# Kernel tuning notes

Hardware: AMD Instinct MI355X
Metric: run time of the kernel (lower is better)

## Reference

```python
import jax, jax.numpy as jnp
import numpy as np

D_K = 8192   # sequence length (module calls it d_k)
D_MODEL = 128

def setup_inputs() -> dict:
    key = jax.random.key(0)
    k1, k2, k3 = jax.random.split(key, 3)
    Q = jax.random.normal(k1, (D_K, D_MODEL), dtype=jnp.float32)
    K = jax.random.normal(k2, (D_K, D_MODEL), dtype=jnp.float32)
    V = jax.random.normal(k3, (D_K, D_MODEL), dtype=jnp.float32)
    return {"Q": Q, "K": K, "V": V}

def reference(Q, K, V):
    # scores: [d_k, d_k] -- full attention matrix, scaled by 1/sqrt(d_k)
    # (faithful to the source: scale uses d_k, the sequence dim)
    inv_scale = 1.0 / jnp.sqrt(jnp.asarray(D_K, dtype=Q.dtype))
    scores = jnp.einsum('qd,kd->qk', Q, K) * inv_scale
    attn = jax.nn.softmax(scores, axis=-1)
    return jnp.einsum('qk,kd->qd', attn, V)
```

## Files before the change

kernel.cpp:

```cpp
#include <hip/hip_runtime.h>

#define SEQ 8192
#define DM  128
#define KS  16

typedef __attribute__((ext_vector_type(8)))  short bf16x8;
typedef __attribute__((ext_vector_type(16))) float f32x16;
typedef __attribute__((ext_vector_type(2)))  unsigned int uintx2;

static __device__ __forceinline__ unsigned short f2bf(float f) {
    unsigned int u = __builtin_bit_cast(unsigned int, f);
    u += 0x7FFFu + ((u >> 16) & 1u);
    return (unsigned short)(u >> 16);
}
static __device__ __forceinline__ unsigned int pack2bf(float a, float b) {
    return ((unsigned int)f2bf(b) << 16) | (unsigned int)f2bf(a);
}
static __device__ __forceinline__ float bflo(unsigned int u) {
    return __builtin_bit_cast(float, u << 16);
}
static __device__ __forceinline__ float bfhi(unsigned int u) {
    return __builtin_bit_cast(float, u & 0xFFFF0000u);
}
static __device__ __forceinline__ bf16x8 as_frag(uint4 v) {
    return __builtin_bit_cast(bf16x8, v);
}
static __device__ __forceinline__ unsigned int pack2bf_trunc(float a, float b) {
    return __builtin_amdgcn_perm(__builtin_bit_cast(unsigned int, b),
                                 __builtin_bit_cast(unsigned int, a), 0x07060302u);
}
static __device__ __forceinline__ void gl_lds16(const void* g, void* l) {
    __builtin_amdgcn_global_load_lds(
        (const __attribute__((address_space(1))) void*)(unsigned long long)g,
        (__attribute__((address_space(3))) void*)(unsigned int)(unsigned long long)l,
        16, 0, 0);
}
#define CL2 (1.4426950408889634f / 90.50966799187809f)

__global__ __launch_bounds__(512) void prep_kernel(
        const float* __restrict__ Q, const float* __restrict__ K,
        const float* __restrict__ V,
        uint2* __restrict__ Qb2, uint4* __restrict__ Kt, uint4* __restrict__ Vt) {
    __shared__ float VL[32 * 132 + 4];
    const int b = blockIdx.x, tid = threadIdx.x;
    const float4* Q4 = (const float4*)Q;
    const float4* K4 = (const float4*)K;
    const float4* V4 = (const float4*)V;

    #pragma unroll
    for (int u = 0; u < 2; ++u) {
        int f4 = u * 512 + tid;
        int k = f4 >> 5, c4 = f4 & 31;
        float4 v = V4[(size_t)b * 1024 + f4];
        *(float4*)(VL + k * 132 + c4 * 4) = v;
    }
    #pragma unroll
    for (int u = 0; u < 2; ++u) {
        int f4 = u * 512 + tid;
        float4 v = Q4[(size_t)b * 1024 + f4];
        Qb2[(size_t)b * 1024 + f4] = make_uint2(pack2bf(v.x * CL2, v.y * CL2),
                                                pack2bf(v.z * CL2, v.w * CL2));
    }
    {
        int p = tid;
        int q = p & 31, h = (p >> 5) & 1, s = p >> 6;
        int fi = (b * 32 + q) * 32 + s * 4 + h * 2;
        float4 a = K4[fi], c = K4[fi + 1];
        Kt[(size_t)b * 512 + p] = make_uint4(pack2bf(a.x, a.y), pack2bf(a.z, a.w),
                                             pack2bf(c.x, c.y), pack2bf(c.z, c.w));
    }
    __syncthreads();
    {
        int p = tid;
        int q = p & 31, h = (p >> 5) & 1, w = p >> 6;
        int d = (w >> 1) * 32 + q;
        int k0 = (w & 1) * 16 + h * 8;
        unsigned int r[4];
        #pragma unroll
        for (int jj = 0; jj < 4; ++jj) {
            float e0 = VL[(k0 + 2 * jj) * 132 + d];
            float e1 = VL[(k0 + 2 * jj + 1) * 132 + d];
            r[jj] = pack2bf(e0, e1);
        }
        Vt[(size_t)b * 512 + p] = make_uint4(r[0], r[1], r[2], r[3]);
    }
}

__global__ __launch_bounds__(256, 2) void attn_kernel(
        const unsigned short* __restrict__ Qb,
        const uint4* __restrict__ Kt,
        const uint4* __restrict__ Vt,
        uint2* __restrict__ Opart, float* __restrict__ Lpart) {
    __shared__ __align__(16) char smem[32768];
    const int tid = threadIdx.x;
    const int wid = tid >> 6, lane = tid & 63;
    const int i = wid;
    const int q = lane & 31, h = lane >> 5;
    const int qt = blockIdx.x & 63, ks = blockIdx.x >> 6;
    const int qbase = qt * 128 + i * 32;
    const int tile0 = ks * 16;

    uint4 qf[8];
    {
        const unsigned short* qrow = Qb + (qbase + q) * DM + 8 * h;
        #pragma unroll
        for (int s = 0; s < 8; ++s) qf[s] = *(const uint4*)(qrow + 16 * s);
    }

    f32x16 oacc[4];
    #pragma unroll
    for (int mb = 0; mb < 4; ++mb)
        #pragma unroll
        for (int r = 0; r < 16; ++r) oacc[mb][r] = 0.f;
    float ls0 = 0.f, ls1 = 0.f, ls2 = 0.f, ls3 = 0.f;

    auto stage = [&](int buf, int tile) {
        char* base = smem + buf * 16384;
        const uint4* kt = Kt + (size_t)tile * 512;
        const uint4* vt = Vt + (size_t)tile * 512;
        #pragma unroll
        for (int u = 0; u < 2; ++u) {
            int ki = i * 2 + u;
            gl_lds16(kt + ki * 64 + lane, base + ki * 1024);
            gl_lds16(vt + ki * 64 + lane, base + 8192 + ki * 1024);
        }
    };

    stage(0, tile0);
    #pragma unroll 1
    for (int t = 0; t < 16; ++t) {
        __syncthreads();
        if (t < 15) stage((t + 1) & 1, tile0 + t + 1);
        const char* kl = smem + (t & 1) * 16384 + lane * 16;

        uint4 kf[8];
        #pragma unroll
        for (int s = 0; s < 8; ++s) kf[s] = *(const uint4*)(kl + s * 1024);

        f32x16 sa, sb;
        #pragma unroll
        for (int r = 0; r < 16; ++r) { sa[r] = 0.f; sb[r] = 0.f; }
        __builtin_amdgcn_s_setprio(1);
        #pragma unroll
        for (int s = 0; s < 4; ++s) {
            sa = __builtin_amdgcn_mfma_f32_32x32x16_bf16(
                     as_frag(kf[s]), as_frag(qf[s]), sa, 0, 0, 0);
            sb = __builtin_amdgcn_mfma_f32_32x32x16_bf16(
                     as_frag(kf[s + 4]), as_frag(qf[s + 4]), sb, 0, 0, 0);
        }
        __builtin_amdgcn_s_setprio(0);

        uint4 vf[8];
        #pragma unroll
        for (int w = 0; w < 8; ++w) vf[w] = *(const uint4*)(kl + 8192 + w * 1024);

        float p[16];
        #pragma unroll
        for (int r = 0; r < 16; ++r) p[r] = __builtin_amdgcn_exp2f(sa[r] + sb[r]);
        #pragma unroll
        for (int r = 0; r < 4; ++r) {
            ls0 += p[4 * r + 0]; ls1 += p[4 * r + 1];
            ls2 += p[4 * r + 2]; ls3 += p[4 * r + 3];
        }
        unsigned int pk[8];
        #pragma unroll
        for (int jj = 0; jj < 8; ++jj) pk[jj] = pack2bf_trunc(p[2 * jj], p[2 * jj + 1]);
        uint4 B0, B1;
        {
            uintx2 r0 = __builtin_amdgcn_permlane32_swap(pk[0], pk[2], false, false);
            uintx2 r1 = __builtin_amdgcn_permlane32_swap(pk[1], pk[3], false, false);
            uintx2 r4 = __builtin_amdgcn_permlane32_swap(pk[4], pk[6], false, false);
            uintx2 r5 = __builtin_amdgcn_permlane32_swap(pk[5], pk[7], false, false);
            B0.x = r0[0];  B0.z = r0[1];
            B0.y = r1[0];  B0.w = r1[1];
            B1.x = r4[0];  B1.z = r4[1];
            B1.y = r5[0];  B1.w = r5[1];
        }

        __builtin_amdgcn_s_setprio(1);
        #pragma unroll
        for (int mb = 0; mb < 4; ++mb) {
            oacc[mb] = __builtin_amdgcn_mfma_f32_32x32x16_bf16(
                           as_frag(vf[mb * 2 + 0]), as_frag(B0), oacc[mb], 0, 0, 0);
            oacc[mb] = __builtin_amdgcn_mfma_f32_32x32x16_bf16(
                           as_frag(vf[mb * 2 + 1]), as_frag(B1), oacc[mb], 0, 0, 0);
        }
        __builtin_amdgcn_s_setprio(0);
    }
    float lsum = (ls0 + ls1) + (ls2 + ls3);

    float l2 = lsum + __shfl_xor(lsum, 32);
    if (h == 0) Lpart[(size_t)ks * SEQ + qbase + q] = l2;

    #pragma unroll
    for (int pass = 0; pass < 2; ++pass) {
        __syncthreads();
        if ((i >> 1) == pass) {
            float* Lg = (float*)(smem + (i & 1) * 16384);
            #pragma unroll
            for (int mb = 0; mb < 4; ++mb)
                #pragma unroll
                for (int r = 0; r < 16; ++r) {
                    int dl = 32 * mb + (r & 3) + 8 * (r >> 2) + 4 * h;
                    Lg[dl * 32 + q] = oacc[mb][r];
                }
        }
        __syncthreads();
        #pragma unroll
        for (int u = 0; u < 8; ++u) {
            int idx = u * 256 + tid;
            int rd = idx >> 4, c4l = idx & 15;
            int ig = c4l >> 3, q4 = c4l & 7;
            float4 v = *(const float4*)(smem + ig * 16384 + (rd * 8 + q4) * 16);
            Opart[(((size_t)(ks * 64 + qt)) * 128 + rd) * 32 + pass * 16 + c4l] =
                make_uint2(pack2bf(v.x, v.y), pack2bf(v.z, v.w));
        }
    }
}

__global__ __launch_bounds__(512) void reduce_kernel(
        const uint2* __restrict__ Opart, const float* __restrict__ Lpart,
        float* __restrict__ Out) {
    __shared__ float T[32 * 132 + 4];
    __shared__ float Rinv[128];
    const int tid = threadIdx.x;
    const int qt = blockIdx.x & 63, dq = blockIdx.x >> 6;
    if (tid < 128) {
        float L = 0.f;
        #pragma unroll
        for (int ks = 0; ks < KS; ++ks) L += Lpart[(size_t)ks * SEQ + qt * 128 + tid];
        Rinv[tid] = 1.0f / L;
    }
    const int c = tid & 31, dsub = tid >> 5;
    float4 acc[2];
    #pragma unroll
    for (int rr = 0; rr < 2; ++rr) { acc[rr].x = acc[rr].y = acc[rr].z = acc[rr].w = 0.f; }
    #pragma unroll
    for (int ks = 0; ks < KS; ++ks) {
        #pragma unroll
        for (int rr = 0; rr < 2; ++rr) {
            int d_l = rr * 16 + dsub;
            uint2 w = Opart[(((size_t)(ks * 64 + qt)) * 128 + dq * 32 + d_l) * 32 + c];
            acc[rr].x += bflo(w.x); acc[rr].y += bfhi(w.x);
            acc[rr].z += bflo(w.y); acc[rr].w += bfhi(w.y);
        }
    }
    #pragma unroll
    for (int rr = 0; rr < 2; ++rr)
        *(float4*)(T + (rr * 16 + dsub) * 132 + c * 4) = acc[rr];
    __syncthreads();
    const int q_l = tid >> 2, part = tid & 3;
    float r = Rinv[q_l];
    #pragma unroll
    for (int g = 0; g < 2; ++g) {
        int d0 = part * 8 + g * 4;
        float4 o;
        o.x = T[(d0 + 0) * 132 + q_l] * r;
        o.y = T[(d0 + 1) * 132 + q_l] * r;
        o.z = T[(d0 + 2) * 132 + q_l] * r;
        o.w = T[(d0 + 3) * 132 + q_l] * r;
        *(float4*)(Out + ((size_t)(qt * 128 + q_l)) * DM + dq * 32 + d0) = o;
    }
}

extern "C" void kernel_launch(void* const* d_in, const int* in_sizes, int n_in,
                              void* d_out, int out_size, void* d_ws, size_t ws_size,
                              hipStream_t stream) {
    const float* Q = (const float*)d_in[0];
    const float* K = (const float*)d_in[1];
    const float* V = (const float*)d_in[2];
    char* ws = (char*)d_ws;
    uint2* Qb2  = (uint2*)ws;
    uint4* Kt   = (uint4*)(ws + 2 * 1024 * 1024);
    uint4* Vt   = (uint4*)(ws + 4 * 1024 * 1024);
    float* Lpart= (float*)(ws + 6 * 1024 * 1024);
    uint2* Opart= (uint2*)(ws + 6 * 1024 * 1024 + 524288);
    float* Out  = (float*)d_out;

    prep_kernel<<<256, 512, 0, stream>>>(Q, K, V, Qb2, Kt, Vt);
    attn_kernel<<<1024, 256, 0, stream>>>((const unsigned short*)Qb2, Kt, Vt,
                                          Opart, Lpart);
    reduce_kernel<<<256, 512, 0, stream>>>(Opart, Lpart, Out);
}
```

Before: 116.7 us.

## Triple-buffer K and double-buffer V with register prefetch of next K tile

Splits the combined K/V staging into separate K (three buffers) and V (two buffers) rings in shared memory, so K is loaded two tiles ahead and V one tile ahead. The next K fragments are read into registers during the current iteration, and the barrier moves to the end of the loop. The aim is to hide global-to-LDS latency and LDS reads behind the MFMA work. In exchange, shared memory grows from 32 KB to 40 KB and register pressure rises, which could reduce occupancy.

New measurement: 119.1 us. +2.1%, slower.

```diff
diff --git a/kernel.cpp b/kernel.cpp
--- a/kernel.cpp
+++ b/kernel.cpp
@@ -91,10 +91,10 @@
         const uint4* __restrict__ Kt,
         const uint4* __restrict__ Vt,
         uint2* __restrict__ Opart, float* __restrict__ Lpart) {
-    __shared__ __align__(16) char smem[32768];
+    __shared__ __align__(16) char smem[40960];
     const int tid = threadIdx.x;
-    const int wid = tid >> 6, lane = tid & 63;
-    const int i = wid;
+    const int lane = tid & 63;
+    const int i = tid >> 6;
     const int q = lane & 31, h = lane >> 5;
     const int qt = blockIdx.x & 63, ks = blockIdx.x >> 6;
     const int qbase = qt * 128 + i * 32;
@@ -114,29 +114,42 @@
         for (int r = 0; r < 16; ++r) oacc[mb][r] = 0.f;
     float ls0 = 0.f, ls1 = 0.f, ls2 = 0.f, ls3 = 0.f;
 
-    auto stage = [&](int buf, int tile) {
-        char* base = smem + buf * 16384;
-        const uint4* kt = Kt + (size_t)tile * 512;
-        const uint4* vt = Vt + (size_t)tile * 512;
+    const uint4* const kt0 = Kt + (size_t)tile0 * 512;
+    const uint4* const vt0 = Vt + (size_t)tile0 * 512;
+
+    auto stageK = [&](int kb, const uint4* src) {
+        char* b = smem + kb * 8192;
         #pragma unroll
         for (int u = 0; u < 2; ++u) {
             int ki = i * 2 + u;
-            gl_lds16(kt + ki * 64 + lane, base + ki * 1024);
-            gl_lds16(vt + ki * 64 + lane, base + 8192 + ki * 1024);
+            gl_lds16(src + ki * 64 + lane, b + ki * 1024);
         }
     };
-
-    stage(0, tile0);
+    auto stageV = [&](int vb, const uint4* src) {
+        char* b = smem + 24576 + vb * 8192;
+        #pragma unroll
+        for (int u = 0; u < 2; ++u) {
+            int ki = i * 2 + u;
+            gl_lds16(src + ki * 64 + lane, b + ki * 1024);
+        }
+    };
+
+    stageK(0, kt0);
+    stageV(0, vt0);
+    stageK(1, kt0 + 512);
+    __syncthreads();
+
+    uint4 kfp[8];
+    #pragma unroll
+    for (int s = 0; s < 8; ++s)
+        kfp[s] = *(const uint4*)(smem + lane * 16 + s * 1024);
+
+    int kb1 = 1;
+    int kb2 = 2;
+    int vb  = 0;
+
     #pragma unroll 1
     for (int t = 0; t < 16; ++t) {
-        __syncthreads();
-        if (t < 15) stage((t + 1) & 1, tile0 + t + 1);
-        const char* kl = smem + (t & 1) * 16384 + lane * 16;
-
-        uint4 kf[8];
-        #pragma unroll
-        for (int s = 0; s < 8; ++s) kf[s] = *(const uint4*)(kl + s * 1024);
-
         f32x16 sa, sb;
         #pragma unroll
         for (int r = 0; r < 16; ++r) { sa[r] = 0.f; sb[r] = 0.f; }
@@ -144,15 +157,26 @@
         #pragma unroll
         for (int s = 0; s < 4; ++s) {
             sa = __builtin_amdgcn_mfma_f32_32x32x16_bf16(
-                     as_frag(kf[s]), as_frag(qf[s]), sa, 0, 0, 0);
+                     as_frag(kfp[s]), as_frag(qf[s]), sa, 0, 0, 0);
             sb = __builtin_amdgcn_mfma_f32_32x32x16_bf16(
-                     as_frag(kf[s + 4]), as_frag(qf[s + 4]), sb, 0, 0, 0);
+                     as_frag(kfp[s + 4]), as_frag(qf[s + 4]), sb, 0, 0, 0);
         }
         __builtin_amdgcn_s_setprio(0);
 
+        if (t < 14) stageK(kb2, kt0 + (size_t)(t + 2) * 512);
+        if (t < 15) stageV(vb ^ 1, vt0 + (size_t)(t + 1) * 512);
+
         uint4 vf[8];
-        #pragma unroll
-        for (int w = 0; w < 8; ++w) vf[w] = *(const uint4*)(kl + 8192 + w * 1024);
+        {
+            const char* vl = smem + 24576 + vb * 8192 + lane * 16;
+            #pragma unroll
+            for (int w = 0; w < 8; ++w) vf[w] = *(const uint4*)(vl + w * 1024);
+        }
+        if (t < 15) {
+            const char* kl = smem + kb1 * 8192 + lane * 16;
+            #pragma unroll
+            for (int s = 0; s < 8; ++s) kfp[s] = *(const uint4*)(kl + s * 1024);
+        }
 
         float p[16];
         #pragma unroll
@@ -186,6 +210,11 @@
                            as_frag(vf[mb * 2 + 1]), as_frag(B1), oacc[mb], 0, 0, 0);
         }
         __builtin_amdgcn_s_setprio(0);
+
+        __syncthreads();
+        kb1 = (kb1 == 2) ? 0 : kb1 + 1;
+        kb2 = (kb2 == 2) ? 0 : kb2 + 1;
+        vb ^= 1;
     }
     float lsum = (ls0 + ls1) + (ls2 + ls3);
 
```

## Load K/V tiles directly into registers with double-buffered prefetch instead of LDS

Applied to the files above, without the earlier changes.

Replaces the global-to-LDS async staging of K and V tiles, and the per-tile __syncthreads, with direct global loads into register arrays. Two register buffers (A/B) alternate, and the next-but-one tile's K and V are prefetched right after they are consumed. This removes LDS round trips and block-wide barriers, but every wave now loads the full K/V tile separately. That raises global/L2 traffic about 4x and raises VGPR pressure, which could hurt occupancy under launch_bounds(256,2).

New measurement: 177.8 us. +52.4%, slower.

```diff
diff --git a/kernel.cpp b/kernel.cpp
--- a/kernel.cpp
+++ b/kernel.cpp
@@ -28,12 +28,6 @@
 static __device__ __forceinline__ unsigned int pack2bf_trunc(float a, float b) {
     return __builtin_amdgcn_perm(__builtin_bit_cast(unsigned int, b),
                                  __builtin_bit_cast(unsigned int, a), 0x07060302u);
-}
-static __device__ __forceinline__ void gl_lds16(const void* g, void* l) {
-    __builtin_amdgcn_global_load_lds(
-        (const __attribute__((address_space(1))) void*)(unsigned long long)g,
-        (__attribute__((address_space(3))) void*)(unsigned int)(unsigned long long)l,
-        16, 0, 0);
 }
 #define CL2 (1.4426950408889634f / 90.50966799187809f)
 
@@ -93,8 +87,8 @@
         uint2* __restrict__ Opart, float* __restrict__ Lpart) {
     __shared__ __align__(16) char smem[32768];
     const int tid = threadIdx.x;
-    const int wid = tid >> 6, lane = tid & 63;
-    const int i = wid;
+    const int lane = tid & 63;
+    const int i = tid >> 6;
     const int q = lane & 31, h = lane >> 5;
     const int qt = blockIdx.x & 63, ks = blockIdx.x >> 6;
     const int qbase = qt * 128 + i * 32;
@@ -114,29 +108,16 @@
         for (int r = 0; r < 16; ++r) oacc[mb][r] = 0.f;
     float ls0 = 0.f, ls1 = 0.f, ls2 = 0.f, ls3 = 0.f;
 
-    auto stage = [&](int buf, int tile) {
-        char* base = smem + buf * 16384;
-        const uint4* kt = Kt + (size_t)tile * 512;
-        const uint4* vt = Vt + (size_t)tile * 512;
-        #pragma unroll
-        for (int u = 0; u < 2; ++u) {
-            int ki = i * 2 + u;
-            gl_lds16(kt + ki * 64 + lane, base + ki * 1024);
-            gl_lds16(vt + ki * 64 + lane, base + 8192 + ki * 1024);
-        }
-    };
-
-    stage(0, tile0);
-    #pragma unroll 1
-    for (int t = 0; t < 16; ++t) {
-        __syncthreads();
-        if (t < 15) stage((t + 1) & 1, tile0 + t + 1);
-        const char* kl = smem + (t & 1) * 16384 + lane * 16;
-
-        uint4 kf[8];
-        #pragma unroll
-        for (int s = 0; s < 8; ++s) kf[s] = *(const uint4*)(kl + s * 1024);
-
+    const uint4* const kp = Kt + (size_t)tile0 * 512 + lane;
+    const uint4* const vp = Vt + (size_t)tile0 * 512 + lane;
+
+    uint4 kA[8], vA[8], kB[8], vB[8];
+    #pragma unroll
+    for (int s = 0; s < 8; ++s) { kA[s] = kp[s * 64];       vA[s] = vp[s * 64]; }
+    #pragma unroll
+    for (int s = 0; s < 8; ++s) { kB[s] = kp[512 + s * 64]; vB[s] = vp[512 + s * 64]; }
+
+    auto tile_body = [&](uint4 (&kX)[8], uint4 (&vX)[8], bool pf, int poff) {
         f32x16 sa, sb;
         #pragma unroll
         for (int r = 0; r < 16; ++r) { sa[r] = 0.f; sb[r] = 0.f; }
@@ -144,16 +125,15 @@
         #pragma unroll
         for (int s = 0; s < 4; ++s) {
             sa = __builtin_amdgcn_mfma_f32_32x32x16_bf16(
-                     as_frag(kf[s]), as_frag(qf[s]), sa, 0, 0, 0);
+                     as_frag(kX[s]), as_frag(qf[s]), sa, 0, 0, 0);
             sb = __builtin_amdgcn_mfma_f32_32x32x16_bf16(
-                     as_frag(kf[s + 4]), as_frag(qf[s + 4]), sb, 0, 0, 0);
+                     as_frag(kX[s + 4]), as_frag(qf[s + 4]), sb, 0, 0, 0);
         }
         __builtin_amdgcn_s_setprio(0);
-
-        uint4 vf[8];
-        #pragma unroll
-        for (int w = 0; w < 8; ++w) vf[w] = *(const uint4*)(kl + 8192 + w * 1024);
-
+        if (pf) {
+            #pragma unroll
+            for (int s = 0; s < 8; ++s) kX[s] = kp[poff + s * 64];
+        }
         float p[16];
         #pragma unroll
         for (int r = 0; r < 16; ++r) p[r] = __builtin_amdgcn_exp2f(sa[r] + sb[r]);
@@ -176,16 +156,25 @@
             B1.x = r4[0];  B1.z = r4[1];
             B1.y = r5[0];  B1.w = r5[1];
         }
-
         __builtin_amdgcn_s_setprio(1);
         #pragma unroll
         for (int mb = 0; mb < 4; ++mb) {
             oacc[mb] = __builtin_amdgcn_mfma_f32_32x32x16_bf16(
-                           as_frag(vf[mb * 2 + 0]), as_frag(B0), oacc[mb], 0, 0, 0);
+                           as_frag(vX[mb * 2 + 0]), as_frag(B0), oacc[mb], 0, 0, 0);
             oacc[mb] = __builtin_amdgcn_mfma_f32_32x32x16_bf16(
-                           as_frag(vf[mb * 2 + 1]), as_frag(B1), oacc[mb], 0, 0, 0);
+                           as_frag(vX[mb * 2 + 1]), as_frag(B1), oacc[mb], 0, 0, 0);
         }
         __builtin_amdgcn_s_setprio(0);
+        if (pf) {
+            #pragma unroll
+            for (int s = 0; s < 8; ++s) vX[s] = vp[poff + s * 64];
+        }
+    };
+
+    #pragma unroll 1
+    for (int t = 0; t < 16; t += 2) {
+        tile_body(kA, vA, t < 14, (t + 2) * 512);
+        tile_body(kB, vB, t < 13, (t + 3) * 512);
     }
     float lsum = (ls0 + ls1) + (ls2 + ls3);
 
```
